# Optimization experiments

Measured on AMD Instinct MI355X. Metric: run time of the kernel, lower is better.

The kernel has to match this reference:

```python
import jax, jax.numpy as jnp
import numpy as np

# dims (must match input_specs / init_kwargs)
B, N, L, D = 4, 2000, 32, 64
H, ND, K, DOUT = 4, 64, 20, 64  # num_heads, node_dim, topk, out_dim
EPS = 1e-8


def setup_inputs() -> dict:
    key = jax.random.key(0)
    ks = jax.random.split(key, 10)
    lim_emb = float(np.sqrt(6.0 / (N + ND)))  # xavier_uniform-ish for embeddings
    lim_l1 = float(np.sqrt(1.0 / H))          # torch Linear default-ish
    lim_l2 = float(np.sqrt(1.0 / (2 * H)))
    lim_w = float(np.sqrt(6.0 / (D + DOUT)))
    return {
        "x": jax.random.normal(ks[0], (B, N, L, D), dtype=jnp.float32),
        "e1": jax.random.uniform(ks[1], (H, N, ND), minval=-lim_emb, maxval=lim_emb, dtype=jnp.float32),
        "e2": jax.random.uniform(ks[2], (H, ND, N), minval=-lim_emb, maxval=lim_emb, dtype=jnp.float32),
        "temperature": jnp.ones((H,), dtype=jnp.float32),
        "ew1": jax.random.uniform(ks[3], (H, 2 * H), minval=-lim_l1, maxval=lim_l1, dtype=jnp.float32),
        "eb1": jax.random.uniform(ks[4], (2 * H,), minval=-lim_l1, maxval=lim_l1, dtype=jnp.float32),
        "ew2": jax.random.uniform(ks[5], (2 * H, 1), minval=-lim_l2, maxval=lim_l2, dtype=jnp.float32),
        "eb2": jax.random.uniform(ks[6], (1,), minval=-lim_l2, maxval=lim_l2, dtype=jnp.float32),
        "weight": jax.random.uniform(ks[7], (D, DOUT), minval=-lim_w, maxval=lim_w, dtype=jnp.float32),
        "bias": jnp.zeros((DOUT,), dtype=jnp.float32),
    }


def _graph_learner(e1, e2, temperature, ew1, eb1, ew2, eb2):
    # per-head scores: (H, N, N)
    scores = jnp.einsum("hnd,hdm->hnm", e1, e2)
    adj = jax.nn.softmax(jax.nn.relu(scores) / temperature[:, None, None], axis=-1)
    # topk sparsification along each row (dim=1 in torch == last axis here)
    _, idx = jax.lax.top_k(adj, K)  # (H, N, K)
    mask = jnp.zeros_like(adj).at[
        jnp.arange(H)[:, None, None], jnp.arange(N)[None, :, None], idx
    ].set(1.0)
    adj = adj * mask
    adj = adj / (jnp.sum(adj, axis=-1, keepdims=True) + EPS)
    # edge encoder MLP over head dim (dropout is identity in eval mode)
    feats = jnp.transpose(adj, (1, 2, 0))              # (N, N, H)
    hid = jax.nn.relu(feats @ ew1 + eb1)               # (N, N, 2H)
    ew = (hid @ ew2 + eb2)[..., 0]                     # (N, N)
    final_adj = jax.nn.sigmoid(ew) * jnp.mean(adj, axis=0)
    return final_adj, adj


def reference(x, e1, e2, temperature, ew1, eb1, ew2, eb2, weight, bias):
    final_adj, _ = _graph_learner(e1, e2, temperature, ew1, eb1, ew2, eb2)
    Bv, Nv, Lv, Dv = x.shape
    xr = jnp.transpose(x, (0, 2, 1, 3)).reshape(Bv * Lv, Nv, Dv)  # (B*L, N, D)
    support = xr @ weight                                          # (B*L, N, Dout)
    # adj.t() @ support  ->  out[b,i,:] = sum_j adj[j,i] * support[b,j,:]
    out = jnp.einsum("ji,bjd->bid", final_adj, support) + bias
    out = jnp.transpose(out.reshape(Bv, Lv, Nv, -1), (0, 2, 1, 3))  # (B, N, L, Dout)
    return out, final_adj
```

## Files before the change

### kernel.cpp

```cpp
#include <hip/hip_runtime.h>

#define NB   2000
#define HH   4
#define KK   20
#define KP   2048
#define GA   4
#define EPSF 1e-8f

typedef unsigned short ushort;
typedef unsigned long long ull;
using short8   = __attribute__((ext_vector_type(8))) short;
using floatx4  = __attribute__((ext_vector_type(4))) float;
using ushortx4 = __attribute__((ext_vector_type(4))) unsigned short;
using ushortx8 = __attribute__((ext_vector_type(8))) unsigned short;

__device__ inline ushort f2bf(float f) {
    unsigned u = __builtin_bit_cast(unsigned, f);
    u += 0x7fffu + ((u >> 16) & 1u);
    return (ushort)(u >> 16);
}

__device__ __forceinline__ void gload_lds16(const ushort* g, ushort* l) {
    __builtin_amdgcn_global_load_lds(
        (const __attribute__((address_space(1))) void*)g,
        (__attribute__((address_space(3))) void*)l, 16, 0, 0);
}

template<int CTRL>
__device__ __forceinline__ float dppmax(float x) {
    int xi = __builtin_bit_cast(int, x);
    int yi = __builtin_amdgcn_update_dpp(xi, xi, CTRL, 0xF, 0xF, false);
    return fmaxf(x, __builtin_bit_cast(float, yi));
}

__device__ __forceinline__ float wavemax63(float x) {
    x = dppmax<0x111>(x);
    x = dppmax<0x112>(x);
    x = dppmax<0x114>(x);
    x = dppmax<0x118>(x);
    x = dppmax<0x142>(x);
    x = dppmax<0x143>(x);
    return x;
}

#define COMP(v,i) ((i)==0?(v).x:(i)==1?(v).y:(i)==2?(v).z:(v).w)

__global__ __launch_bounds__(256) void k_scores_topk(
    const float* __restrict__ e1, const float* __restrict__ e2,
    const float* __restrict__ temperature,
    int* __restrict__ topk_idx, float* __restrict__ topk_val)
{
    const int h  = blockIdx.y;
    const int n0 = blockIdx.x * GA;
    const int t  = threadIdx.x;
    const int w  = t >> 6, lane = t & 63;

    __shared__ float e1s[GA][64];
    __shared__ float red[GA][4];
    __shared__ ull   lists[4][GA][KK + 1];
    __shared__ float selpv[GA][KK];
    __shared__ int   seli[GA][KK];
    __shared__ float ssum[GA];

    e1s[t >> 6][t & 63] = e1[(size_t)(h * NB + n0 + (t >> 6)) * 64 + (t & 63)];
    __syncthreads();

    const float rtemp = 1.f / temperature[h];
    const float* __restrict__ e2h = e2 + (size_t)h * 64 * NB;

    const int  mbase = w * 512 + lane * 8;
    const bool valid = (mbase < NB);
    const int  mload = valid ? mbase : (NB - 8);

    float acc[GA][8];
#pragma unroll
    for (int r = 0; r < GA; r++)
#pragma unroll
        for (int k = 0; k < 8; k++) acc[r][k] = 0.f;

    for (int d4 = 0; d4 < 64; d4 += 4) {
        float4 ev0 = *(const float4*)&e1s[0][d4];
        float4 ev1 = *(const float4*)&e1s[1][d4];
        float4 ev2 = *(const float4*)&e1s[2][d4];
        float4 ev3 = *(const float4*)&e1s[3][d4];
#pragma unroll
        for (int dd = 0; dd < 4; dd++) {
            const float* __restrict__ row = e2h + (size_t)(d4 + dd) * NB + mload;
            float4 a = *(const float4*)row;
            float4 b = *(const float4*)(row + 4);
            float f0 = COMP(ev0, dd), f1 = COMP(ev1, dd);
            float f2 = COMP(ev2, dd), f3 = COMP(ev3, dd);
            acc[0][0] += f0*a.x; acc[0][1] += f0*a.y; acc[0][2] += f0*a.z; acc[0][3] += f0*a.w;
            acc[0][4] += f0*b.x; acc[0][5] += f0*b.y; acc[0][6] += f0*b.z; acc[0][7] += f0*b.w;
            acc[1][0] += f1*a.x; acc[1][1] += f1*a.y; acc[1][2] += f1*a.z; acc[1][3] += f1*a.w;
            acc[1][4] += f1*b.x; acc[1][5] += f1*b.y; acc[1][6] += f1*b.z; acc[1][7] += f1*b.w;
            acc[2][0] += f2*a.x; acc[2][1] += f2*a.y; acc[2][2] += f2*a.z; acc[2][3] += f2*a.w;
            acc[2][4] += f2*b.x; acc[2][5] += f2*b.y; acc[2][6] += f2*b.z; acc[2][7] += f2*b.w;
            acc[3][0] += f3*a.x; acc[3][1] += f3*a.y; acc[3][2] += f3*a.z; acc[3][3] += f3*a.w;
            acc[3][4] += f3*b.x; acc[3][5] += f3*b.y; acc[3][6] += f3*b.z; acc[3][7] += f3*b.w;
        }
    }

#pragma unroll
    for (int r = 0; r < GA; r++) {
        float tvm = -1.f;
#pragma unroll
        for (int k = 0; k < 8; k++) {
            float v = valid ? fmaxf(acc[r][k], 0.f) * rtemp : -1.f;
            acc[r][k] = v;
            tvm = fmaxf(tvm, v);
        }
        tvm = wavemax63(tvm);
        if (lane == 63) red[r][w] = tvm;
    }

    float lm[GA]; int ak[GA];
#pragma unroll
    for (int r = 0; r < GA; r++) {
        float l = acc[r][0]; int a = 0;
#pragma unroll
        for (int k = 1; k < 8; k++)
            if (acc[r][k] > l) { l = acc[r][k]; a = k; }
        lm[r] = l; ak[r] = a;
    }

    for (int round = 0; round < KK; round++) {
        float M[GA];
#pragma unroll
        for (int r = 0; r < GA; r++) M[r] = lm[r];
#pragma unroll
        for (int r = 0; r < GA; r++) M[r] = dppmax<0x111>(M[r]);
#pragma unroll
        for (int r = 0; r < GA; r++) M[r] = dppmax<0x112>(M[r]);
#pragma unroll
        for (int r = 0; r < GA; r++) M[r] = dppmax<0x114>(M[r]);
#pragma unroll
        for (int r = 0; r < GA; r++) M[r] = dppmax<0x118>(M[r]);
#pragma unroll
        for (int r = 0; r < GA; r++) M[r] = dppmax<0x142>(M[r]);
#pragma unroll
        for (int r = 0; r < GA; r++) M[r] = dppmax<0x143>(M[r]);
#pragma unroll
        for (int r = 0; r < GA; r++)
            M[r] = __builtin_bit_cast(float,
                     __builtin_amdgcn_readlane(__builtin_bit_cast(int, M[r]), 63));
#pragma unroll
        for (int r = 0; r < GA; r++) {
            ull ball = __ballot(lm[r] == M[r]);
            int wl   = __ffsll(ball) - 1;
            if (lane == wl) {
                int gidx = mbase + ak[r];
                lists[w][r][round] =
                    ((ull)__float_as_uint(M[r]) << 32) | (unsigned)~gidx;
#pragma unroll
                for (int k = 0; k < 8; k++) if (k == ak[r]) acc[r][k] = -2.f;
                float l = acc[r][0]; int a = 0;
#pragma unroll
                for (int k = 1; k < 8; k++)
                    if (acc[r][k] > l) { l = acc[r][k]; a = k; }
                lm[r] = l; ak[r] = a;
            }
        }
    }
#pragma unroll
    for (int r = 0; r < GA; r++)
        if (lane == 0) lists[w][r][KK] = 0ULL;
    __syncthreads();

    if (t < GA) {
        const int r = t;
        float mx = fmaxf(fmaxf(red[r][0], red[r][1]), fmaxf(red[r][2], red[r][3]));
        int p0 = 0, p1 = 0, p2 = 0, p3 = 0;
        ull h0 = lists[0][r][0], h1 = lists[1][r][0];
        ull h2 = lists[2][r][0], h3 = lists[3][r][0];
        float ss = 0.f;
        for (int q = 0; q < KK; q++) {
            ull a_ = h0 >= h1 ? h0 : h1; int wa = h0 >= h1 ? 0 : 1;
            ull b_ = h2 >= h3 ? h2 : h3; int wb = h2 >= h3 ? 2 : 3;
            ull bk = a_ >= b_ ? a_ : b_; int bw = a_ >= b_ ? wa : wb;
            float tvv = __uint_as_float((unsigned)(bk >> 32));
            float pv  = __expf(tvv - mx);
            selpv[r][q] = pv;
            seli[r][q]  = (int)~(unsigned)bk;
            ss += pv;
            if      (bw == 0) h0 = lists[0][r][++p0];
            else if (bw == 1) h1 = lists[1][r][++p1];
            else if (bw == 2) h2 = lists[2][r][++p2];
            else              h3 = lists[3][r][++p3];
        }
        ssum[r] = ss;
    }
    __syncthreads();

    if (t < GA * KK) {
        int r = t / KK, q = t % KK;
        int o = (h * NB + n0 + r) * KK + q;
        topk_idx[o] = seli[r][q];
        topk_val[o] = selpv[r][q] / (ssum[r] + EPSF);
    }
}

__global__ __launch_bounds__(256) void k_final_adj(
    const int* __restrict__ topk_idx, const float* __restrict__ topk_val,
    const float* __restrict__ ew1, const float* __restrict__ eb1,
    const float* __restrict__ ew2, const float* __restrict__ eb2,
    float* __restrict__ fadj_out, ushort* __restrict__ faT_b)
{
    const int i = blockIdx.x;
    const int t = threadIdx.x;

    __shared__ float rows[HH][NB];
    __shared__ float w1[32];
    __shared__ float b1[8];
    __shared__ float w2[8];
    __shared__ float b2v;

    for (int k = t; k < HH * NB; k += 256) ((float*)rows)[k] = 0.f;
    if (t < 32) w1[t] = ew1[t];
    if (t < 8)  { b1[t] = eb1[t]; w2[t] = ew2[t]; }
    if (t == 0) b2v = eb2[0];
    __syncthreads();

    if (t < HH * KK) {
        int h = t / KK, r = t % KK;
        int o = (h * NB + i) * KK + r;
        rows[h][topk_idx[o]] = topk_val[o];
    }
    __syncthreads();

#pragma unroll
    for (int k = 0; k < 8; k++) {
        int j = k * 256 + t;
        if (j < NB) {
            float f0 = rows[0][j], f1 = rows[1][j], f2 = rows[2][j], f3 = rows[3][j];
            float mean = (f0 + f1 + f2 + f3) * 0.25f;
            float outv = 0.f;
            if (mean > 0.f) {
                float ewv = b2v;
#pragma unroll
                for (int c = 0; c < 8; c++) {
                    float hid = f0 * w1[c] + f1 * w1[8 + c] + f2 * w1[16 + c] + f3 * w1[24 + c] + b1[c];
                    hid = fmaxf(hid, 0.f);
                    ewv += hid * w2[c];
                }
                float sig = 1.f / (1.f + expf(-ewv));
                outv = sig * mean;
                faT_b[(size_t)j * KP + i] = f2bf(outv);
            }
            fadj_out[(size_t)i * NB + j] = outv;
        }
    }
}

__global__ __launch_bounds__(256) void k_support(
    const float* __restrict__ x, const float* __restrict__ w,
    ushort* __restrict__ S_b)
{
    const int j = blockIdx.x;
    const int t = threadIdx.x;

    __shared__ float xs[128 * 65];
    __shared__ float ws[64 * 64];

    for (int k = t; k < 4096; k += 256) ws[k] = w[k];
    for (int idx = t; idx < 8192; idx += 256) {
        int b_ = idx >> 11, rem = idx & 2047;
        int bl = (b_ << 5) + (rem >> 6), dd = rem & 63;
        xs[bl * 65 + dd] = x[(size_t)b_ * 4096000 + (size_t)j * 2048 + rem];
    }
    __syncthreads();

    const int dq = t & 15;
    const int g  = t >> 4;
    float acc[8][4];
#pragma unroll
    for (int r = 0; r < 8; r++)
#pragma unroll
        for (int c = 0; c < 4; c++) acc[r][c] = 0.f;

    for (int dd = 0; dd < 64; dd++) {
        float4 w4 = *(const float4*)&ws[dd * 64 + dq * 4];
#pragma unroll
        for (int r = 0; r < 8; r++) {
            float xv = xs[(g * 8 + r) * 65 + dd];
            acc[r][0] += xv * w4.x;
            acc[r][1] += xv * w4.y;
            acc[r][2] += xv * w4.z;
            acc[r][3] += xv * w4.w;
        }
    }

#pragma unroll
    for (int r = 0; r < 8; r++) {
        int bl = g * 8 + r;
        ushortx4 v;
        v.x = f2bf(acc[r][0]); v.y = f2bf(acc[r][1]);
        v.z = f2bf(acc[r][2]); v.w = f2bf(acc[r][3]);
        *(ushortx4*)&S_b[(size_t)j * 8192 + bl * 64 + dq * 4] = v;
    }
}

__global__ __launch_bounds__(256) void k_transpose(
    const ushort* __restrict__ S_b, ushort* __restrict__ ST)
{
    const int jt = blockIdx.x;
    const int ct = blockIdx.y;
    const int t  = threadIdx.x;

    __shared__ ushort tile[64 * 65];

#pragma unroll
    for (int p = 0; p < 4; p++) {
        int q = p * 256 + t;
        int row = q >> 4, seg = q & 15;
        int j = jt * 64 + row;
        ushort v0 = 0, v1 = 0, v2 = 0, v3 = 0;
        if (j < NB) {
            const ushort* src = &S_b[(size_t)j * 8192 + ct * 64 + seg * 4];
            v0 = src[0]; v1 = src[1]; v2 = src[2]; v3 = src[3];
        }
        ushort* dst = &tile[row * 65 + seg * 4];
        dst[0] = v0; dst[1] = v1; dst[2] = v2; dst[3] = v3;
    }
    __syncthreads();

#pragma unroll
    for (int p = 0; p < 2; p++) {
        int q = p * 256 + t;
        int rc = q >> 3, s = q & 7;
        ushortx8 o;
#pragma unroll
        for (int k = 0; k < 8; k++) o[k] = tile[(s * 8 + k) * 65 + rc];
        *(ushortx8*)&ST[(size_t)(ct * 64 + rc) * KP + jt * 64 + s * 8] = o;
    }
}

__global__ __launch_bounds__(256) void k_gemm(
    const ushort* __restrict__ A, const ushort* __restrict__ B,
    const float* __restrict__ bias, float* __restrict__ out)
{
    __shared__ ushort As[128 * 64];
    __shared__ ushort Bs[128 * 64];

    const int t    = threadIdx.x;
    const int lane = t & 63, wave = t >> 6;
    const int wm   = wave & 1, wn = wave >> 1;
    const int i0   = blockIdx.x * 128;
    const int c0   = blockIdx.y * 128;

    const int lr = lane >> 3;
    const int dg = lane & 7;

    floatx4 acc[4][4];
#pragma unroll
    for (int r = 0; r < 4; r++)
#pragma unroll
        for (int c = 0; c < 4; c++) acc[r][c] = (floatx4)(0.f);

    for (int kb = 0; kb < 32; kb++) {
        __syncthreads();
#pragma unroll
        for (int p = 0; p < 4; p++) {
            int rowb = p * 32 + wave * 8;
            int row  = rowb + lr;
            int g    = dg ^ lr;
            const ushort* ga = &A[(size_t)(i0 + row) * KP + kb * 64 + g * 8];
            const ushort* gb = &B[(size_t)(c0 + row) * KP + kb * 64 + g * 8];
            gload_lds16(ga, &As[rowb * 64]);
            gload_lds16(gb, &Bs[rowb * 64]);
        }
        __syncthreads();

#pragma unroll
        for (int kk = 0; kk < 2; kk++) {
            short8 af[4], bf[4];
            const int gidx = kk * 4 + (lane >> 4);
            const int dsw  = gidx ^ (lane & 7);
#pragma unroll
            for (int r = 0; r < 4; r++) {
                int m = wm * 64 + r * 16 + (lane & 15);
                af[r] = *(const short8*)&As[m * 64 + dsw * 8];
            }
#pragma unroll
            for (int c = 0; c < 4; c++) {
                int m = wn * 64 + c * 16 + (lane & 15);
                bf[c] = *(const short8*)&Bs[m * 64 + dsw * 8];
            }
#pragma unroll
            for (int r = 0; r < 4; r++)
#pragma unroll
                for (int c = 0; c < 4; c++)
                    acc[r][c] = __builtin_amdgcn_mfma_f32_16x16x32_bf16(af[r], bf[c], acc[r][c], 0, 0, 0);
        }
    }

    const int mq = (lane >> 4) * 4;
    const int nn = lane & 15;
#pragma unroll
    for (int r = 0; r < 4; r++) {
#pragma unroll
        for (int c = 0; c < 4; c++) {
            int cg = c0 + wn * 64 + c * 16 + nn;
            float bv = bias[cg & 63];
            int b_ = cg >> 11, rem = cg & 2047;
            float* op = out + (size_t)b_ * 4096000 + rem;
#pragma unroll
            for (int rg = 0; rg < 4; rg++) {
                int i = i0 + wm * 64 + r * 16 + mq + rg;
                if (i < NB) op[(size_t)i * 2048] = acc[r][c][rg] + bv;
            }
        }
    }
}

extern "C" void kernel_launch(void* const* d_in, const int* in_sizes, int n_in,
                              void* d_out, int out_size, void* d_ws, size_t ws_size,
                              hipStream_t stream)
{
    const float* x           = (const float*)d_in[0];
    const float* e1          = (const float*)d_in[1];
    const float* e2          = (const float*)d_in[2];
    const float* temperature = (const float*)d_in[3];
    const float* ew1         = (const float*)d_in[4];
    const float* eb1         = (const float*)d_in[5];
    const float* ew2         = (const float*)d_in[6];
    const float* eb2         = (const float*)d_in[7];
    const float* weight      = (const float*)d_in[8];
    const float* bias        = (const float*)d_in[9];

    float* out  = (float*)d_out;
    float* fadj = out + 16384000;

    ushort* ST       = (ushort*)d_ws;
    ushort* S_b      = ST + (size_t)8192 * KP;
    ushort* faT_b    = (ushort*)((char*)d_ws + 66322432u);
    int*    topk_idx = (int*)(faT_b + (size_t)KP * KP);
    float*  topk_val = (float*)(topk_idx + 160000);

    hipMemsetAsync(faT_b, 0, (size_t)KP * KP * sizeof(ushort), stream);

    k_scores_topk<<<dim3(NB / GA, HH), 256, 0, stream>>>(e1, e2, temperature,
                                                         topk_idx, topk_val);
    k_final_adj<<<NB, 256, 0, stream>>>(topk_idx, topk_val, ew1, eb1, ew2, eb2,
                                        fadj, faT_b);
    k_support<<<NB, 256, 0, stream>>>(x, weight, S_b);
    k_transpose<<<dim3(32, 128), 256, 0, stream>>>(S_b, ST);
    k_gemm<<<dim3(16, 64), 256, 0, stream>>>(faT_b, ST, bias, out);
}
```

Measured before the change: 417.2 us.

## Split score GEMV across 8 waves and stage scores through LDS for top-k

The scores/top-k kernel now launches 512 threads per block. All 8 waves compute the e1·e2 dot products with 4 columns per lane, then write them to a new 32 KB shared-memory score buffer. After a barrier, the first 4 waves reload 8 scores per lane and run the unchanged relu/scale, max and top-k selection. The intent is to double the parallelism and latency hiding of the memory-bound score computation. In exchange it adds LDS traffic, an extra barrier and a large shared allocation that may cut the number of resident blocks.

```diff
diff --git a/kernel.cpp b/kernel.cpp
--- a/kernel.cpp
+++ b/kernel.cpp
@@ -45,7 +45,7 @@
 
 #define COMP(v,i) ((i)==0?(v).x:(i)==1?(v).y:(i)==2?(v).z:(v).w)
 
-__global__ __launch_bounds__(256) void k_scores_topk(
+__global__ __launch_bounds__(512) void k_scores_topk(
     const float* __restrict__ e1, const float* __restrict__ e2,
     const float* __restrict__ temperature,
     int* __restrict__ topk_idx, float* __restrict__ topk_val)
@@ -56,115 +56,133 @@
     const int w  = t >> 6, lane = t & 63;
 
     __shared__ float e1s[GA][64];
+    __shared__ float scoresS[GA][2048];
     __shared__ float red[GA][4];
     __shared__ ull   lists[4][GA][KK + 1];
     __shared__ float selpv[GA][KK];
     __shared__ int   seli[GA][KK];
     __shared__ float ssum[GA];
 
-    e1s[t >> 6][t & 63] = e1[(size_t)(h * NB + n0 + (t >> 6)) * 64 + (t & 63)];
+    if (t < 256)
+        e1s[t >> 6][t & 63] = e1[(size_t)(h * NB + n0 + (t >> 6)) * 64 + (t & 63)];
     __syncthreads();
 
     const float rtemp = 1.f / temperature[h];
     const float* __restrict__ e2h = e2 + (size_t)h * 64 * NB;
 
-    const int  mbase = w * 512 + lane * 8;
-    const bool valid = (mbase < NB);
-    const int  mload = valid ? mbase : (NB - 8);
-
-    float acc[GA][8];
-#pragma unroll
-    for (int r = 0; r < GA; r++)
-#pragma unroll
-        for (int k = 0; k < 8; k++) acc[r][k] = 0.f;
-
-    for (int d4 = 0; d4 < 64; d4 += 4) {
-        float4 ev0 = *(const float4*)&e1s[0][d4];
-        float4 ev1 = *(const float4*)&e1s[1][d4];
-        float4 ev2 = *(const float4*)&e1s[2][d4];
-        float4 ev3 = *(const float4*)&e1s[3][d4];
-#pragma unroll
-        for (int dd = 0; dd < 4; dd++) {
-            const float* __restrict__ row = e2h + (size_t)(d4 + dd) * NB + mload;
-            float4 a = *(const float4*)row;
-            float4 b = *(const float4*)(row + 4);
-            float f0 = COMP(ev0, dd), f1 = COMP(ev1, dd);
-            float f2 = COMP(ev2, dd), f3 = COMP(ev3, dd);
-            acc[0][0] += f0*a.x; acc[0][1] += f0*a.y; acc[0][2] += f0*a.z; acc[0][3] += f0*a.w;
-            acc[0][4] += f0*b.x; acc[0][5] += f0*b.y; acc[0][6] += f0*b.z; acc[0][7] += f0*b.w;
-            acc[1][0] += f1*a.x; acc[1][1] += f1*a.y; acc[1][2] += f1*a.z; acc[1][3] += f1*a.w;
-            acc[1][4] += f1*b.x; acc[1][5] += f1*b.y; acc[1][6] += f1*b.z; acc[1][7] += f1*b.w;
-            acc[2][0] += f2*a.x; acc[2][1] += f2*a.y; acc[2][2] += f2*a.z; acc[2][3] += f2*a.w;
-            acc[2][4] += f2*b.x; acc[2][5] += f2*b.y; acc[2][6] += f2*b.z; acc[2][7] += f2*b.w;
-            acc[3][0] += f3*a.x; acc[3][1] += f3*a.y; acc[3][2] += f3*a.z; acc[3][3] += f3*a.w;
-            acc[3][4] += f3*b.x; acc[3][5] += f3*b.y; acc[3][6] += f3*b.z; acc[3][7] += f3*b.w;
-        }
-    }
-
-#pragma unroll
-    for (int r = 0; r < GA; r++) {
-        float tvm = -1.f;
-#pragma unroll
-        for (int k = 0; k < 8; k++) {
-            float v = valid ? fmaxf(acc[r][k], 0.f) * rtemp : -1.f;
-            acc[r][k] = v;
-            tvm = fmaxf(tvm, v);
-        }
-        tvm = wavemax63(tvm);
-        if (lane == 63) red[r][w] = tvm;
-    }
-
-    float lm[GA]; int ak[GA];
-#pragma unroll
-    for (int r = 0; r < GA; r++) {
-        float l = acc[r][0]; int a = 0;
-#pragma unroll
-        for (int k = 1; k < 8; k++)
-            if (acc[r][k] > l) { l = acc[r][k]; a = k; }
-        lm[r] = l; ak[r] = a;
-    }
-
-    for (int round = 0; round < KK; round++) {
-        float M[GA];
-#pragma unroll
-        for (int r = 0; r < GA; r++) M[r] = lm[r];
-#pragma unroll
-        for (int r = 0; r < GA; r++) M[r] = dppmax<0x111>(M[r]);
-#pragma unroll
-        for (int r = 0; r < GA; r++) M[r] = dppmax<0x112>(M[r]);
-#pragma unroll
-        for (int r = 0; r < GA; r++) M[r] = dppmax<0x114>(M[r]);
-#pragma unroll
-        for (int r = 0; r < GA; r++) M[r] = dppmax<0x118>(M[r]);
-#pragma unroll
-        for (int r = 0; r < GA; r++) M[r] = dppmax<0x142>(M[r]);
-#pragma unroll
-        for (int r = 0; r < GA; r++) M[r] = dppmax<0x143>(M[r]);
+    {
+        const int mb1 = w * 256 + lane * 4;
+        const int ml1 = (mb1 < NB) ? mb1 : (NB - 4);
+
+        float acc[GA][4];
 #pragma unroll
         for (int r = 0; r < GA; r++)
-            M[r] = __builtin_bit_cast(float,
-                     __builtin_amdgcn_readlane(__builtin_bit_cast(int, M[r]), 63));
+#pragma unroll
+            for (int c = 0; c < 4; c++) acc[r][c] = 0.f;
+
+        for (int d4 = 0; d4 < 64; d4 += 4) {
+            float4 ev0 = *(const float4*)&e1s[0][d4];
+            float4 ev1 = *(const float4*)&e1s[1][d4];
+            float4 ev2 = *(const float4*)&e1s[2][d4];
+            float4 ev3 = *(const float4*)&e1s[3][d4];
+#pragma unroll
+            for (int dd = 0; dd < 4; dd++) {
+                float4 a = *(const float4*)(e2h + (size_t)(d4 + dd) * NB + ml1);
+                float f0 = COMP(ev0, dd), f1 = COMP(ev1, dd);
+                float f2 = COMP(ev2, dd), f3 = COMP(ev3, dd);
+                acc[0][0] += f0*a.x; acc[0][1] += f0*a.y; acc[0][2] += f0*a.z; acc[0][3] += f0*a.w;
+                acc[1][0] += f1*a.x; acc[1][1] += f1*a.y; acc[1][2] += f1*a.z; acc[1][3] += f1*a.w;
+                acc[2][0] += f2*a.x; acc[2][1] += f2*a.y; acc[2][2] += f2*a.z; acc[2][3] += f2*a.w;
+                acc[3][0] += f3*a.x; acc[3][1] += f3*a.y; acc[3][2] += f3*a.z; acc[3][3] += f3*a.w;
+            }
+        }
+
 #pragma unroll
         for (int r = 0; r < GA; r++) {
-            ull ball = __ballot(lm[r] == M[r]);
-            int wl   = __ffsll(ball) - 1;
-            if (lane == wl) {
-                int gidx = mbase + ak[r];
-                lists[w][r][round] =
-                    ((ull)__float_as_uint(M[r]) << 32) | (unsigned)~gidx;
-#pragma unroll
-                for (int k = 0; k < 8; k++) if (k == ak[r]) acc[r][k] = -2.f;
-                float l = acc[r][0]; int a = 0;
-#pragma unroll
-                for (int k = 1; k < 8; k++)
-                    if (acc[r][k] > l) { l = acc[r][k]; a = k; }
-                lm[r] = l; ak[r] = a;
-            }
-        }
-    }
-#pragma unroll
-    for (int r = 0; r < GA; r++)
-        if (lane == 0) lists[w][r][KK] = 0ULL;
+            float4 v; v.x = acc[r][0]; v.y = acc[r][1]; v.z = acc[r][2]; v.w = acc[r][3];
+            *(float4*)&scoresS[r][mb1] = v;
+        }
+    }
+    __syncthreads();
+
+    if (w < 4) {
+        const int  mbase = w * 512 + lane * 8;
+        const bool valid = (mbase < NB);
+
+        float acc[GA][8];
+#pragma unroll
+        for (int r = 0; r < GA; r++) {
+            float4 lo = *(const float4*)&scoresS[r][mbase];
+            float4 hi = *(const float4*)&scoresS[r][mbase + 4];
+            acc[r][0] = lo.x; acc[r][1] = lo.y; acc[r][2] = lo.z; acc[r][3] = lo.w;
+            acc[r][4] = hi.x; acc[r][5] = hi.y; acc[r][6] = hi.z; acc[r][7] = hi.w;
+        }
+
+#pragma unroll
+        for (int r = 0; r < GA; r++) {
+            float tvm = -1.f;
+#pragma unroll
+            for (int k = 0; k < 8; k++) {
+                float v = valid ? fmaxf(acc[r][k], 0.f) * rtemp : -1.f;
+                acc[r][k] = v;
+                tvm = fmaxf(tvm, v);
+            }
+            tvm = wavemax63(tvm);
+            if (lane == 63) red[r][w] = tvm;
+        }
+
+        float lm[GA]; int ak[GA];
+#pragma unroll
+        for (int r = 0; r < GA; r++) {
+            float l = acc[r][0]; int a = 0;
+#pragma unroll
+            for (int k = 1; k < 8; k++)
+                if (acc[r][k] > l) { l = acc[r][k]; a = k; }
+            lm[r] = l; ak[r] = a;
+        }
+
+        for (int round = 0; round < KK; round++) {
+            float M[GA];
+#pragma unroll
+            for (int r = 0; r < GA; r++) M[r] = lm[r];
+#pragma unroll
+            for (int r = 0; r < GA; r++) M[r] = dppmax<0x111>(M[r]);
+#pragma unroll
+            for (int r = 0; r < GA; r++) M[r] = dppmax<0x112>(M[r]);
+#pragma unroll
+            for (int r = 0; r < GA; r++) M[r] = dppmax<0x114>(M[r]);
+#pragma unroll
+            for (int r = 0; r < GA; r++) M[r] = dppmax<0x118>(M[r]);
+#pragma unroll
+            for (int r = 0; r < GA; r++) M[r] = dppmax<0x142>(M[r]);
+#pragma unroll
+            for (int r = 0; r < GA; r++) M[r] = dppmax<0x143>(M[r]);
+#pragma unroll
+            for (int r = 0; r < GA; r++)
+                M[r] = __builtin_bit_cast(float,
+                         __builtin_amdgcn_readlane(__builtin_bit_cast(int, M[r]), 63));
+#pragma unroll
+            for (int r = 0; r < GA; r++) {
+                ull ball = __ballot(lm[r] == M[r]);
+                int wl   = __ffsll(ball) - 1;
+                if (lane == wl) {
+                    int gidx = mbase + ak[r];
+                    lists[w][r][round] =
+                        ((ull)__float_as_uint(M[r]) << 32) | (unsigned)~gidx;
+#pragma unroll
+                    for (int k = 0; k < 8; k++) if (k == ak[r]) acc[r][k] = -2.f;
+                    float l = acc[r][0]; int a = 0;
+#pragma unroll
+                    for (int k = 1; k < 8; k++)
+                        if (acc[r][k] > l) { l = acc[r][k]; a = k; }
+                    lm[r] = l; ak[r] = a;
+                }
+            }
+        }
+#pragma unroll
+        for (int r = 0; r < GA; r++)
+            if (lane == 0) lists[w][r][KK] = 0ULL;
+    }
     __syncthreads();
 
     if (t < GA) {
@@ -439,7 +457,7 @@
 
     hipMemsetAsync(faT_b, 0, (size_t)KP * KP * sizeof(ushort), stream);
 
-    k_scores_topk<<<dim3(NB / GA, HH), 256, 0, stream>>>(e1, e2, temperature,
+    k_scores_topk<<<dim3(NB / GA, HH), 512, 0, stream>>>(e1, e2, temperature,
                                                          topk_idx, topk_val);
     k_final_adj<<<NB, 256, 0, stream>>>(topk_idx, topk_val, ew1, eb1, ew2, eb2,
                                         fadj, faT_b);
```

New measurement: 393.8 us. 5.6% less time.
